# Performance work log

Measured on AMD Instinct MI355X. Metric: run time of the kernel, lower is better.

## Reference

```python
import jax, jax.numpy as jnp
import numpy as np

NEG_SLOPE = 0.2
STRONG_CONVEXITY = 0.5


def _scalar(x, Wq, Wl, bl, Wz, wz_out, wq_out, wl_out):
    # x: [B, D]; Wq/Wl: [L, H, D]; bl: [L, H]; Wz: [L-1, H, H]
    # Precompute all per-layer x-dependent terms in two batched einsums.
    qx = jnp.einsum('lhd,bd->lbh', Wq, x) ** 2          # [L, B, H]
    lx = jnp.einsum('lhd,bd->lbh', Wl, x) + bl[:, None, :]  # [L, B, H]
    z = jax.nn.leaky_relu(qx[0] + lx[0], negative_slope=NEG_SLOPE)

    def step(z, inputs):
        W, q, l = inputs
        z = jax.nn.leaky_relu(z @ W.T + q + l, negative_slope=NEG_SLOPE)
        return z, None

    z, _ = jax.lax.scan(step, z, (Wz, qx[1:], lx[1:]))
    # Final layer to scalar output (no bias on last wx_lin per torch code).
    out = z @ wz_out.T + (x @ wq_out.T) ** 2 + x @ wl_out.T  # [B, 1]
    return out


def setup_inputs() -> dict:
    key = jax.random.key(0)
    ks = jax.random.split(key, 8)
    B, D, H, L = 8192, 128, 512, 10
    f32 = jnp.float32
    x = jax.random.normal(ks[0], (B, D), f32)
    Wq = jax.random.normal(ks[1], (L, H, D), f32) * (1.0 / np.sqrt(D))
    Wl = jax.random.normal(ks[2], (L, H, D), f32) * (1.0 / np.sqrt(D))
    bl = jax.random.normal(ks[3], (L, H), f32) * 0.01
    # wz weights are kept non-negative in the original (clamp/exp init)
    Wz = jnp.abs(jax.random.normal(ks[4], (L - 1, H, H), f32)) * (1.0 / np.sqrt(H))
    wz_out = jnp.abs(jax.random.normal(ks[5], (1, H), f32)) * (1.0 / np.sqrt(H))
    wq_out = jax.random.normal(ks[6], (1, D), f32) * (1.0 / np.sqrt(D))
    wl_out = jax.random.normal(ks[7], (1, D), f32) * (1.0 / np.sqrt(D))
    return {"x": x, "Wq": Wq, "Wl": Wl, "bl": bl, "Wz": Wz,
            "wz_out": wz_out, "wq_out": wq_out, "wl_out": wl_out}


def reference(x, Wq, Wl, bl, Wz, wz_out, wq_out, wl_out):
    # forward = (1 - mu) * d(scalar)/dx + mu * x, with grad_outputs = ones
    def scalar_sum(xx):
        return jnp.sum(_scalar(xx, Wq, Wl, bl, Wz, wz_out, wq_out, wl_out))

    gx = jax.grad(scalar_sum)(x)  # per-sample gradient, [B, D]
    return (1.0 - STRONG_CONVEXITY) * gx + STRONG_CONVEXITY * x
```

## Files before the change

### kernel.cpp

```cpp
#include <hip/hip_runtime.h>


#define Bn 8192
#define Dn 128
#define Hn 512
#define Ln 10
#define NW (Ln * Hn)

constexpr float NS = 0.2f;

typedef __attribute__((ext_vector_type(8))) short short8;
typedef __attribute__((ext_vector_type(4))) float f32x4;

typedef const __attribute__((address_space(1))) void GV;
typedef __attribute__((address_space(3))) void LV;

__device__ __forceinline__ void gload16(const void* g, void* l) {
    __builtin_amdgcn_global_load_lds((GV*)g, (LV*)l, 16, 0, 0);
}

#define MFMA(acc, a, b) acc = __builtin_amdgcn_mfma_f32_16x16x32_bf16(a, b, acc, 0, 0, 0)

__device__ __forceinline__ unsigned short bf16_rne(float v) {
    unsigned u = __float_as_uint(v);
    u += 0x7FFFu + ((u >> 16) & 1u);
    return (unsigned short)(u >> 16);
}
__device__ __forceinline__ float bf2f(unsigned short h) {
    return __uint_as_float(((unsigned)h) << 16);
}
__device__ __forceinline__ void split2(float v, unsigned short& h, unsigned short& l) {
    h = bf16_rne(v);
    l = bf16_rne(v - bf2f(h));
}


__global__ __launch_bounds__(256) void split_flat(const float* __restrict__ in,
        unsigned short* __restrict__ hi, unsigned short* __restrict__ lo, int n4) {
    int i = blockIdx.x * 256 + threadIdx.x;
    if (i >= n4) return;
    float4 v = ((const float4*)in)[i];
    ushort4 h, l;
    split2(v.x, h.x, l.x);
    split2(v.y, h.y, l.y);
    split2(v.z, h.z, l.z);
    split2(v.w, h.w, l.w);
    ((ushort4*)hi)[i] = h;
    ((ushort4*)lo)[i] = l;
}

__global__ __launch_bounds__(256) void transpose_split(const float* __restrict__ in,
        unsigned short* __restrict__ hi, unsigned short* __restrict__ lo, int R, int C) {
    __shared__ float t[32][33];
    const size_t off = (size_t)blockIdx.z * R * C;
    const float* src = in + off;
    unsigned short* dh = hi + off;
    unsigned short* dl = lo + off;
    const int r0 = blockIdx.x * 32, c0 = blockIdx.y * 32;
    const int tr = threadIdx.x >> 5, tc = threadIdx.x & 31;
#pragma unroll
    for (int i = 0; i < 4; ++i)
        t[tr + 8 * i][tc] = src[(size_t)(r0 + tr + 8 * i) * C + c0 + tc];
    __syncthreads();
#pragma unroll
    for (int i = 0; i < 4; ++i) {
        float v = t[tc][tr + 8 * i];
        unsigned short h, l; split2(v, h, l);
        size_t o = (size_t)(c0 + tr + 8 * i) * R + r0 + tc;
        dh[o] = h; dl[o] = l;
    }
}


__global__ __launch_bounds__(256) void gemm_uall(
    const unsigned short* __restrict__ xh, const unsigned short* __restrict__ xl,
    const unsigned short* __restrict__ Wh, const unsigned short* __restrict__ Wv,
    float* __restrict__ u)
{
    __shared__ __align__(16) char smem[32768];
    unsigned short* Ah = (unsigned short*)smem;
    unsigned short* Al = (unsigned short*)(smem + 8192);
    unsigned short* Bh = (unsigned short*)(smem + 16384);
    unsigned short* Bl = (unsigned short*)(smem + 24576);

    const int tid = threadIdx.x;
    const int w = tid >> 6, lane = tid & 63;
    const int lq = lane >> 4, lc = lane & 15;
    const int wm = (w & 1) * 64, wn = (w >> 1) * 64;
    const int row0 = blockIdx.x * 128, col0 = blockIdx.y * 128;
    const int sr = lane >> 2, sk = (lane & 3) * 8;

    f32x4 acc[4][4];
#pragma unroll
    for (int i = 0; i < 4; ++i)
#pragma unroll
        for (int j = 0; j < 4; ++j)
#pragma unroll
            for (int r = 0; r < 4; ++r) acc[i][j][r] = 0.f;

    for (int k0 = 0; k0 < Dn; k0 += 32) {
        __syncthreads();
        for (int c = w; c < 8; c += 4) {
            size_t ga_ = (size_t)(row0 + c * 16 + sr) * Dn + k0 + sk;
            gload16(xh + ga_, Ah + c * 512);
            gload16(xl + ga_, Al + c * 512);
            size_t gb = (size_t)(col0 + c * 16 + sr) * Dn + k0 + sk;
            gload16(Wh + gb, Bh + c * 512);
            gload16(Wv + gb, Bl + c * 512);
        }
        __syncthreads();
        short8 ah[4], al[4];
#pragma unroll
        for (int mt = 0; mt < 4; ++mt) {
            int ao = (wm + mt * 16 + lc) * 32 + lq * 8;
            ah[mt] = *(const short8*)(Ah + ao);
            al[mt] = *(const short8*)(Al + ao);
        }
#pragma unroll
        for (int nt = 0; nt < 4; ++nt) {
            int bo = (wn + nt * 16 + lc) * 32 + lq * 8;
            short8 bh = *(const short8*)(Bh + bo);
            short8 bv = *(const short8*)(Bl + bo);
#pragma unroll
            for (int mt = 0; mt < 4; ++mt) {
                MFMA(acc[mt][nt], ah[mt], bh);
                MFMA(acc[mt][nt], ah[mt], bv);
                MFMA(acc[mt][nt], al[mt], bh);
            }
        }
    }

#pragma unroll
    for (int nt = 0; nt < 4; ++nt) {
        const int col = col0 + wn + nt * 16 + lc;
#pragma unroll
        for (int mt = 0; mt < 4; ++mt) {
            const int rowb = row0 + wm + mt * 16;
#pragma unroll
            for (int r = 0; r < 4; ++r)
                u[(size_t)(rowb + lq * 4 + r) * NW + col] = acc[mt][nt][r];
        }
    }
}


__global__ __launch_bounds__(256) void fwd_mfma(
    const unsigned short* __restrict__ xh, const unsigned short* __restrict__ xl,
    const unsigned short* __restrict__ zph, const unsigned short* __restrict__ zpl,
    const unsigned short* __restrict__ Wzh, const unsigned short* __restrict__ Wzl,
    const unsigned short* __restrict__ Wlh, const unsigned short* __restrict__ Wll,
    const float* __restrict__ bl,
    const float* __restrict__ u,
    unsigned short* __restrict__ zoh, unsigned short* __restrict__ zol,
    unsigned short* __restrict__ mask16, int hasZ)
{
    __shared__ __align__(16) char smem[16384];
    unsigned short* Ah = (unsigned short*)smem;
    unsigned short* Al = (unsigned short*)(smem + 4096);
    unsigned short* Bh = (unsigned short*)(smem + 8192);
    unsigned short* Bl = (unsigned short*)(smem + 12288);

    const int tid = threadIdx.x;
    const int w = tid >> 6, lane = tid & 63;
    const int lq = lane >> 4, lc = lane & 15;
    const int wm = (w & 1) * 32, wn = (w >> 1) * 32;
    const int row0 = blockIdx.x * 64, col0 = blockIdx.y * 64;
    const int sr = lane >> 2, sk = (lane & 3) * 8;

    f32x4 acc[2][2];
#pragma unroll
    for (int i = 0; i < 2; ++i)
#pragma unroll
        for (int j = 0; j < 2; ++j)
#pragma unroll
            for (int r = 0; r < 4; ++r) acc[i][j][r] = 0.f;

    if (hasZ) {
        for (int k0 = 0; k0 < Hn; k0 += 32) {
            __syncthreads();
            {
                size_t ga_ = (size_t)(row0 + w * 16 + sr) * Hn + k0 + sk;
                size_t gb  = (size_t)(col0 + w * 16 + sr) * Hn + k0 + sk;
                gload16(zph + ga_, Ah + w * 512);
                gload16(zpl + ga_, Al + w * 512);
                gload16(Wzh + gb, Bh + w * 512);
                gload16(Wzl + gb, Bl + w * 512);
            }
            __syncthreads();
            short8 ah[2], al[2];
#pragma unroll
            for (int mt = 0; mt < 2; ++mt) {
                int ao = (wm + mt * 16 + lc) * 32 + lq * 8;
                ah[mt] = *(const short8*)(Ah + ao);
                al[mt] = *(const short8*)(Al + ao);
            }
#pragma unroll
            for (int nt = 0; nt < 2; ++nt) {
                int bo = (wn + nt * 16 + lc) * 32 + lq * 8;
                short8 bh = *(const short8*)(Bh + bo);
                short8 bv = *(const short8*)(Bl + bo);
#pragma unroll
                for (int mt = 0; mt < 2; ++mt) {
                    MFMA(acc[mt][nt], ah[mt], bh);
                    MFMA(acc[mt][nt], ah[mt], bv);
                    MFMA(acc[mt][nt], al[mt], bh);
                }
            }
        }
    }

    for (int k0 = 0; k0 < Dn; k0 += 32) {
        __syncthreads();
        {
            size_t ga_ = (size_t)(row0 + w * 16 + sr) * Dn + k0 + sk;
            size_t gb  = (size_t)(col0 + w * 16 + sr) * Dn + k0 + sk;
            gload16(xh + ga_, Ah + w * 512);
            gload16(xl + ga_, Al + w * 512);
            gload16(Wlh + gb, Bh + w * 512);
            gload16(Wll + gb, Bl + w * 512);
        }
        __syncthreads();
        short8 ah[2], al[2];
#pragma unroll
        for (int mt = 0; mt < 2; ++mt) {
            int ao = (wm + mt * 16 + lc) * 32 + lq * 8;
            ah[mt] = *(const short8*)(Ah + ao);
            al[mt] = *(const short8*)(Al + ao);
        }
#pragma unroll
        for (int nt = 0; nt < 2; ++nt) {
            int bo = (wn + nt * 16 + lc) * 32 + lq * 8;
            short8 bh = *(const short8*)(Bh + bo);
            short8 bv = *(const short8*)(Bl + bo);
#pragma unroll
            for (int mt = 0; mt < 2; ++mt) {
                MFMA(acc[mt][nt], ah[mt], bh);
                MFMA(acc[mt][nt], ah[mt], bv);
                MFMA(acc[mt][nt], al[mt], bh);
            }
        }
    }

#pragma unroll
    for (int nt = 0; nt < 2; ++nt) {
        const int colb = col0 + wn + nt * 16;
        const int col = colb + lc;
        const float blv = bl[col];
#pragma unroll
        for (int mt = 0; mt < 2; ++mt) {
            const int rowb = row0 + wm + mt * 16;
#pragma unroll
            for (int r = 0; r < 4; ++r) {
                const int row = rowb + lq * 4 + r;
                float uq = u[(size_t)row * NW + col];
                float pre = acc[mt][nt][r] + uq * uq + blv;
                bool m = pre >= 0.f;
                unsigned long long bal = __ballot(m);
                if (lc == 0) {
                    mask16[(size_t)row * 32 + (colb >> 4)] =
                        (unsigned short)((bal >> (lq * 16)) & 0xFFFFull);
                }
                float zv = m ? pre : NS * pre;
                unsigned short h, l; split2(zv, h, l);
                size_t o = (size_t)row * Hn + col;
                zoh[o] = h; zol[o] = l;
            }
        }
    }
}


__global__ __launch_bounds__(256) void bwd_g_mfma(
    const unsigned short* __restrict__ gah, const unsigned short* __restrict__ gal,
    const unsigned short* __restrict__ WzTh, const unsigned short* __restrict__ WzTl,
    const unsigned short* __restrict__ maskprev,
    const float* __restrict__ u,
    unsigned short* __restrict__ goh, unsigned short* __restrict__ gol,
    unsigned short* __restrict__ a1h, unsigned short* __restrict__ a1l)
{
    __shared__ __align__(16) char smem[16384];
    unsigned short* Ah = (unsigned short*)smem;
    unsigned short* Al = (unsigned short*)(smem + 4096);
    unsigned short* Bh = (unsigned short*)(smem + 8192);
    unsigned short* Bl = (unsigned short*)(smem + 12288);

    const int tid = threadIdx.x;
    const int w = tid >> 6, lane = tid & 63;
    const int lq = lane >> 4, lc = lane & 15;
    const int wm = (w & 1) * 32, wn = (w >> 1) * 32;
    const int row0 = blockIdx.x * 64, col0 = blockIdx.y * 64;
    const int sr = lane >> 2, sk = (lane & 3) * 8;

    f32x4 acc[2][2];
#pragma unroll
    for (int i = 0; i < 2; ++i)
#pragma unroll
        for (int j = 0; j < 2; ++j)
#pragma unroll
            for (int r = 0; r < 4; ++r) acc[i][j][r] = 0.f;

    for (int k0 = 0; k0 < Hn; k0 += 32) {
        __syncthreads();
        {
            size_t ga_ = (size_t)(row0 + w * 16 + sr) * Hn + k0 + sk;
            size_t gb  = (size_t)(col0 + w * 16 + sr) * Hn + k0 + sk;
            gload16(gah + ga_, Ah + w * 512);
            gload16(gal + ga_, Al + w * 512);
            gload16(WzTh + gb, Bh + w * 512);
            gload16(WzTl + gb, Bl + w * 512);
        }
        __syncthreads();
        short8 ah[2], al[2];
#pragma unroll
        for (int mt = 0; mt < 2; ++mt) {
            int ao = (wm + mt * 16 + lc) * 32 + lq * 8;
            ah[mt] = *(const short8*)(Ah + ao);
            al[mt] = *(const short8*)(Al + ao);
        }
#pragma unroll
        for (int nt = 0; nt < 2; ++nt) {
            int bo = (wn + nt * 16 + lc) * 32 + lq * 8;
            short8 bh = *(const short8*)(Bh + bo);
            short8 bv = *(const short8*)(Bl + bo);
#pragma unroll
            for (int mt = 0; mt < 2; ++mt) {
                MFMA(acc[mt][nt], ah[mt], bh);
                MFMA(acc[mt][nt], ah[mt], bv);
                MFMA(acc[mt][nt], al[mt], bh);
            }
        }
    }

#pragma unroll
    for (int nt = 0; nt < 2; ++nt) {
        const int colb = col0 + wn + nt * 16;
        const int col = colb + lc;
#pragma unroll
        for (int mt = 0; mt < 2; ++mt) {
            const int rowb = row0 + wm + mt * 16;
#pragma unroll
            for (int r = 0; r < 4; ++r) {
                int row = rowb + lq * 4 + r;
                unsigned short wbits = maskprev[(size_t)row * 32 + (colb >> 4)];
                float f = ((wbits >> lc) & 1) ? 1.f : NS;
                float v = acc[mt][nt][r] * f;
                unsigned short h, l; split2(v, h, l);
                size_t o = (size_t)row * Hn + col;
                goh[o] = h; gol[o] = l;
                float uv = u[(size_t)row * NW + col];
                float a1 = 2.f * uv * v;
                split2(a1, h, l);
                a1h[o] = h; a1l[o] = l;
            }
        }
    }
}


__global__ __launch_bounds__(256) void bwd_x_mfma(
    const unsigned short* __restrict__ a1h, const unsigned short* __restrict__ a1l,
    const unsigned short* __restrict__ a2h, const unsigned short* __restrict__ a2l,
    const unsigned short* __restrict__ WqTh, const unsigned short* __restrict__ WqTl,
    const unsigned short* __restrict__ WlTh, const unsigned short* __restrict__ WlTl,
    float* __restrict__ gxs)
{
    __shared__ __align__(16) char smem[32768];
    unsigned short* A1h = (unsigned short*)smem;
    unsigned short* A1l = (unsigned short*)(smem + 4096);
    unsigned short* A2h = (unsigned short*)(smem + 8192);
    unsigned short* A2l = (unsigned short*)(smem + 12288);
    unsigned short* Bqh = (unsigned short*)(smem + 16384);
    unsigned short* Bql = (unsigned short*)(smem + 20480);
    unsigned short* Blh = (unsigned short*)(smem + 24576);
    unsigned short* Bll = (unsigned short*)(smem + 28672);

    const int tid = threadIdx.x;
    const int w = tid >> 6, lane = tid & 63;
    const int lq = lane >> 4, lc = lane & 15;
    const int wm = (w & 1) * 32, wn = (w >> 1) * 32;
    const int row0 = blockIdx.x * 64, col0 = blockIdx.y * 64;
    const int kb = blockIdx.z * 256;
    float* gx = gxs + (size_t)blockIdx.z * Bn * Dn;
    const int str = tid >> 2, stk = (tid & 3) * 8;

    f32x4 acc[2][2];
#pragma unroll
    for (int i = 0; i < 2; ++i)
#pragma unroll
        for (int j = 0; j < 2; ++j)
#pragma unroll
            for (int r = 0; r < 4; ++r) acc[i][j][r] = 0.f;

    for (int k0 = kb; k0 < kb + 256; k0 += 32) {
        __syncthreads();
        {
            size_t ga_ = (size_t)(row0 + str) * Hn + k0 + stk;
            size_t gb = (size_t)(col0 + str) * Hn + k0 + stk;
            int lo_ = str * 32 + stk;
            gload16(a1h + ga_, A1h + lo_);
            gload16(a1l + ga_, A1l + lo_);
            gload16(a2h + ga_, A2h + lo_);
            gload16(a2l + ga_, A2l + lo_);
            gload16(WqTh + gb, Bqh + lo_);
            gload16(WqTl + gb, Bql + lo_);
            gload16(WlTh + gb, Blh + lo_);
            gload16(WlTl + gb, Bll + lo_);
        }
        __syncthreads();
        short8 f1h[2], f1l[2], f2h[2], f2l[2];
#pragma unroll
        for (int mt = 0; mt < 2; ++mt) {
            int ao = (wm + mt * 16 + lc) * 32 + lq * 8;
            f1h[mt] = *(const short8*)(A1h + ao);
            f1l[mt] = *(const short8*)(A1l + ao);
            f2h[mt] = *(const short8*)(A2h + ao);
            f2l[mt] = *(const short8*)(A2l + ao);
        }
#pragma unroll
        for (int nt = 0; nt < 2; ++nt) {
            int bo = (wn + nt * 16 + lc) * 32 + lq * 8;
            short8 qh = *(const short8*)(Bqh + bo);
            short8 ql_ = *(const short8*)(Bql + bo);
            short8 lh = *(const short8*)(Blh + bo);
            short8 ll_ = *(const short8*)(Bll + bo);
#pragma unroll
            for (int mt = 0; mt < 2; ++mt) {
                MFMA(acc[mt][nt], f1h[mt], qh);
                MFMA(acc[mt][nt], f1h[mt], ql_);
                MFMA(acc[mt][nt], f1l[mt], qh);
                MFMA(acc[mt][nt], f2h[mt], lh);
                MFMA(acc[mt][nt], f2h[mt], ll_);
                MFMA(acc[mt][nt], f2l[mt], lh);
            }
        }
    }

#pragma unroll
    for (int nt = 0; nt < 2; ++nt) {
        const int col = col0 + wn + nt * 16 + lc;
#pragma unroll
        for (int mt = 0; mt < 2; ++mt) {
            const int rowb = row0 + wm + mt * 16;
#pragma unroll
            for (int r = 0; r < 4; ++r) {
                size_t o = (size_t)(rowb + lq * 4 + r) * Dn + col;
                gx[o] += acc[mt][nt][r];
            }
        }
    }
}


__global__ __launch_bounds__(256) void zero_buf(float* __restrict__ p, int n4) {
    int i = blockIdx.x * 256 + threadIdx.x;
    if (i < n4) ((float4*)p)[i] = make_float4(0.f, 0.f, 0.f, 0.f);
}

__global__ __launch_bounds__(256) void ga_init(
    const float* __restrict__ wz_out, const unsigned short* __restrict__ mask9,
    const float* __restrict__ u9,
    unsigned short* __restrict__ gh, unsigned short* __restrict__ gl,
    unsigned short* __restrict__ a1h, unsigned short* __restrict__ a1l)
{
    int i = blockIdx.x * 256 + threadIdx.x;
    int e = i << 2;
    int b = e >> 9, h = e & 511;
    unsigned short wbits = mask9[(size_t)b * 32 + (h >> 4)];
    float4 wv = *(const float4*)(wz_out + h);
    float4 uv = *(const float4*)(u9 + (size_t)b * NW + h);
    int sh = h & 15;
    ushort4 oh, ol, th, tl;
    float f;
    f = wv.x * (((wbits >> (sh + 0)) & 1) ? 1.f : NS); split2(f, oh.x, ol.x); split2(2.f * uv.x * f, th.x, tl.x);
    f = wv.y * (((wbits >> (sh + 1)) & 1) ? 1.f : NS); split2(f, oh.y, ol.y); split2(2.f * uv.y * f, th.y, tl.y);
    f = wv.z * (((wbits >> (sh + 2)) & 1) ? 1.f : NS); split2(f, oh.z, ol.z); split2(2.f * uv.z * f, th.z, tl.z);
    f = wv.w * (((wbits >> (sh + 3)) & 1) ? 1.f : NS); split2(f, oh.w, ol.w); split2(2.f * uv.w * f, th.w, tl.w);
    *(ushort4*)(gh + e) = oh;
    *(ushort4*)(gl + e) = ol;
    *(ushort4*)(a1h + e) = th;
    *(ushort4*)(a1l + e) = tl;
}

__global__ __launch_bounds__(256) void rowdot_kernel(
    const float* __restrict__ x, const float* __restrict__ wq_out, float* __restrict__ s) {
    const int b = blockIdx.x * 4 + (threadIdx.x >> 6);
    const int lane = threadIdx.x & 63;
    float v = x[(size_t)b * Dn + lane] * wq_out[lane] +
              x[(size_t)b * Dn + 64 + lane] * wq_out[64 + lane];
#pragma unroll
    for (int off = 32; off > 0; off >>= 1) v += __shfl_down(v, off, 64);
    if (lane == 0) s[b] = v;
}

__global__ __launch_bounds__(256) void final_kernel(
    float* __restrict__ out, const float* __restrict__ gxs,
    const float* __restrict__ x, const float* __restrict__ s,
    const float* __restrict__ wq_out, const float* __restrict__ wl_out) {
    const int i = blockIdx.x * 256 + threadIdx.x;
    const int base = i << 2;
    const int b = base >> 7;
    const int d = base & (Dn - 1);
    float4 g0 = *(const float4*)(gxs + base);
    float4 g1 = *(const float4*)(gxs + (size_t)Bn * Dn + base);
    float4 xv = *(const float4*)(x + base);
    float4 wq = *(const float4*)(wq_out + d);
    float4 wl = *(const float4*)(wl_out + d);
    const float sb = s[b];
    float4 o;
    o.x = 0.5f * (g0.x + g1.x) + sb * wq.x + 0.5f * wl.x + 0.5f * xv.x;
    o.y = 0.5f * (g0.y + g1.y) + sb * wq.y + 0.5f * wl.y + 0.5f * xv.y;
    o.z = 0.5f * (g0.z + g1.z) + sb * wq.z + 0.5f * wl.z + 0.5f * xv.z;
    o.w = 0.5f * (g0.w + g1.w) + sb * wq.w + 0.5f * wl.w + 0.5f * xv.w;
    *(float4*)(out + base) = o;
}


extern "C" void kernel_launch(void* const* d_in, const int* in_sizes, int n_in,
                              void* d_out, int out_size, void* d_ws, size_t ws_size,
                              hipStream_t stream) {
    (void)in_sizes; (void)n_in; (void)out_size; (void)ws_size;
    const float* x      = (const float*)d_in[0];
    const float* Wq     = (const float*)d_in[1];
    const float* Wl     = (const float*)d_in[2];
    const float* bl     = (const float*)d_in[3];
    const float* Wz     = (const float*)d_in[4];
    const float* wz_out = (const float*)d_in[5];
    const float* wq_out = (const float*)d_in[6];
    const float* wl_out = (const float*)d_in[7];
    float* out = (float*)d_out;

    char* p = (char*)d_ws;
    #define CARVE(name, bytes) unsigned short* name = (unsigned short*)p; p += (((size_t)(bytes)) + 255) & ~(size_t)255;
    CARVE(xh,  (size_t)Bn*Dn*2)  CARVE(xl,  (size_t)Bn*Dn*2)
    CARVE(Wqh, (size_t)Ln*Hn*Dn*2) CARVE(Wql, (size_t)Ln*Hn*Dn*2)
    CARVE(Wlh, (size_t)Ln*Hn*Dn*2) CARVE(Wll, (size_t)Ln*Hn*Dn*2)
    CARVE(WqTh,(size_t)Ln*Hn*Dn*2) CARVE(WqTl,(size_t)Ln*Hn*Dn*2)
    CARVE(WlTh,(size_t)Ln*Hn*Dn*2) CARVE(WlTl,(size_t)Ln*Hn*Dn*2)
    CARVE(Wzh, (size_t)(Ln-1)*Hn*Hn*2) CARVE(Wzl, (size_t)(Ln-1)*Hn*Hn*2)
    CARVE(WzTh,(size_t)(Ln-1)*Hn*Hn*2) CARVE(WzTl,(size_t)(Ln-1)*Hn*Hn*2)
    CARVE(zAh, (size_t)Bn*Hn*2) CARVE(zAl, (size_t)Bn*Hn*2)
    CARVE(zBh, (size_t)Bn*Hn*2) CARVE(zBl, (size_t)Bn*Hn*2)
    CARVE(a1h, (size_t)Bn*Hn*2) CARVE(a1l, (size_t)Bn*Hn*2)
    CARVE(mask16, (size_t)Ln*Bn*32*2)
    float* s = (float*)p; p += (size_t)Bn*4 + 256;
    float* gxs = (float*)p; p += (size_t)2*Bn*Dn*4;
    float* uall = (float*)p; p += (size_t)Bn*NW*4;
    #undef CARVE

    split_flat<<<(Bn*Dn/4 + 255)/256, 256, 0, stream>>>(x, xh, xl, Bn*Dn/4);
    split_flat<<<(Ln*Hn*Dn/4 + 255)/256, 256, 0, stream>>>(Wq, Wqh, Wql, Ln*Hn*Dn/4);
    split_flat<<<(Ln*Hn*Dn/4 + 255)/256, 256, 0, stream>>>(Wl, Wlh, Wll, Ln*Hn*Dn/4);
    split_flat<<<((Ln-1)*Hn*Hn/4 + 255)/256, 256, 0, stream>>>(Wz, Wzh, Wzl, (Ln-1)*Hn*Hn/4);
    transpose_split<<<dim3(Hn/32, Dn/32, Ln), 256, 0, stream>>>(Wq, WqTh, WqTl, Hn, Dn);
    transpose_split<<<dim3(Hn/32, Dn/32, Ln), 256, 0, stream>>>(Wl, WlTh, WlTl, Hn, Dn);
    transpose_split<<<dim3(Hn/32, Hn/32, Ln-1), 256, 0, stream>>>(Wz, WzTh, WzTl, Hn, Hn);

    rowdot_kernel<<<Bn/4, 256, 0, stream>>>(x, wq_out, s);
    zero_buf<<<(2*Bn*Dn/4 + 255)/256, 256, 0, stream>>>(gxs, 2*Bn*Dn/4);

    gemm_uall<<<dim3(Bn/128, NW/128), 256, 0, stream>>>(xh, xl, Wqh, Wql, uall);

    const dim3 gF(Bn/64, Hn/64);

    fwd_mfma<<<gF, 256, 0, stream>>>(xh, xl, nullptr, nullptr, nullptr, nullptr,
        Wlh, Wll, bl, uall, zAh, zAl, mask16, 0);
    for (int l = 1; l < Ln; ++l) {
        const unsigned short* zh  = (l & 1) ? zAh : zBh;
        const unsigned short* zl_ = (l & 1) ? zAl : zBl;
        unsigned short* oh  = (l & 1) ? zBh : zAh;
        unsigned short* ol_ = (l & 1) ? zBl : zAl;
        fwd_mfma<<<gF, 256, 0, stream>>>(xh, xl, zh, zl_,
            Wzh + (size_t)(l-1)*Hn*Hn, Wzl + (size_t)(l-1)*Hn*Hn,
            Wlh + (size_t)l*Hn*Dn, Wll + (size_t)l*Hn*Dn,
            bl + (size_t)l*Hn, uall + (size_t)l*Hn,
            oh, ol_, mask16 + (size_t)l*Bn*32, 1);
    }

    ga_init<<<(Bn*Hn/4)/256, 256, 0, stream>>>(wz_out, mask16 + (size_t)9*Bn*32,
        uall + (size_t)9*Hn, zAh, zAl, a1h, a1l);

    for (int l = Ln - 1; l >= 0; --l) {
        int sidx = (Ln - 1 - l) & 1;
        const unsigned short* gh_ = sidx ? zBh : zAh;
        const unsigned short* gl_ = sidx ? zBl : zAl;
        bwd_x_mfma<<<dim3(Bn/64, Dn/64, 2), 256, 0, stream>>>(
            a1h, a1l, gh_, gl_,
            WqTh + (size_t)l*Dn*Hn, WqTl + (size_t)l*Dn*Hn,
            WlTh + (size_t)l*Dn*Hn, WlTl + (size_t)l*Dn*Hn, gxs);
        if (l > 0) {
            unsigned short* oh  = sidx ? zAh : zBh;
            unsigned short* ol_ = sidx ? zAl : zBl;
            bwd_g_mfma<<<gF, 256, 0, stream>>>(gh_, gl_,
                WzTh + (size_t)(l-1)*Hn*Hn, WzTl + (size_t)(l-1)*Hn*Hn,
                mask16 + (size_t)(l-1)*Bn*32,
                uall + (size_t)(l-1)*Hn,
                oh, ol_, a1h, a1l);
        }
    }

    final_kernel<<<(Bn*Dn/4)/256, 256, 0, stream>>>(out, gxs, x, s, wq_out, wl_out);
}
```

Measured before the change: 999.0 us.

## Double-buffer LDS tiles in MFMA kernels and skip unused final-layer z writes

Converts the forward, backward-g and backward-x MFMA GEMM loops to a double-buffered LDS scheme. The next K-slice is prefetched with global_load_lds while the current slice is consumed, which drops one barrier per iteration. It also adds a writeZ flag so the last forward layer writes only the mask and skips its z output, which nothing reads. Shared memory per block doubles (up to 64KB in bwd_x), which may lower occupancy. Correctness now relies on the single barrier per iteration being enough for the buffer reuse.

```diff
diff --git a/kernel.cpp b/kernel.cpp
--- a/kernel.cpp
+++ b/kernel.cpp
@@ -152,20 +152,17 @@
     const float* __restrict__ bl,
     const float* __restrict__ u,
     unsigned short* __restrict__ zoh, unsigned short* __restrict__ zol,
-    unsigned short* __restrict__ mask16, int hasZ)
+    unsigned short* __restrict__ mask16, int hasZ, int writeZ)
 {
-    __shared__ __align__(16) char smem[16384];
-    unsigned short* Ah = (unsigned short*)smem;
-    unsigned short* Al = (unsigned short*)(smem + 4096);
-    unsigned short* Bh = (unsigned short*)(smem + 8192);
-    unsigned short* Bl = (unsigned short*)(smem + 12288);
-
+    __shared__ __align__(16) char smem[32768];
+    unsigned short* base = (unsigned short*)smem;
     const int tid = threadIdx.x;
     const int w = tid >> 6, lane = tid & 63;
     const int lq = lane >> 4, lc = lane & 15;
     const int wm = (w & 1) * 32, wn = (w >> 1) * 32;
     const int row0 = blockIdx.x * 64, col0 = blockIdx.y * 64;
     const int sr = lane >> 2, sk = (lane & 3) * 8;
+    const int lA = w * 512;
 
     f32x4 acc[2][2];
 #pragma unroll
@@ -176,29 +173,40 @@
             for (int r = 0; r < 4; ++r) acc[i][j][r] = 0.f;
 
     if (hasZ) {
+        {
+            unsigned short* S = base;
+            size_t ga_ = (size_t)(row0 + w * 16 + sr) * Hn + sk;
+            size_t gb  = (size_t)(col0 + w * 16 + sr) * Hn + sk;
+            gload16(zph + ga_, S + lA);
+            gload16(zpl + ga_, S + 2048 + lA);
+            gload16(Wzh + gb, S + 4096 + lA);
+            gload16(Wzl + gb, S + 6144 + lA);
+        }
+        int cur = 0;
         for (int k0 = 0; k0 < Hn; k0 += 32) {
             __syncthreads();
-            {
-                size_t ga_ = (size_t)(row0 + w * 16 + sr) * Hn + k0 + sk;
-                size_t gb  = (size_t)(col0 + w * 16 + sr) * Hn + k0 + sk;
-                gload16(zph + ga_, Ah + w * 512);
-                gload16(zpl + ga_, Al + w * 512);
-                gload16(Wzh + gb, Bh + w * 512);
-                gload16(Wzl + gb, Bl + w * 512);
-            }
-            __syncthreads();
+            if (k0 + 32 < Hn) {
+                unsigned short* S = base + (cur ^ 1) * 8192;
+                size_t ga_ = (size_t)(row0 + w * 16 + sr) * Hn + k0 + 32 + sk;
+                size_t gb  = (size_t)(col0 + w * 16 + sr) * Hn + k0 + 32 + sk;
+                gload16(zph + ga_, S + lA);
+                gload16(zpl + ga_, S + 2048 + lA);
+                gload16(Wzh + gb, S + 4096 + lA);
+                gload16(Wzl + gb, S + 6144 + lA);
+            }
+            unsigned short* S = base + cur * 8192;
             short8 ah[2], al[2];
 #pragma unroll
             for (int mt = 0; mt < 2; ++mt) {
                 int ao = (wm + mt * 16 + lc) * 32 + lq * 8;
-                ah[mt] = *(const short8*)(Ah + ao);
-                al[mt] = *(const short8*)(Al + ao);
+                ah[mt] = *(const short8*)(S + ao);
+                al[mt] = *(const short8*)(S + 2048 + ao);
             }
 #pragma unroll
             for (int nt = 0; nt < 2; ++nt) {
                 int bo = (wn + nt * 16 + lc) * 32 + lq * 8;
-                short8 bh = *(const short8*)(Bh + bo);
-                short8 bv = *(const short8*)(Bl + bo);
+                short8 bh = *(const short8*)(S + 4096 + bo);
+                short8 bv = *(const short8*)(S + 6144 + bo);
 #pragma unroll
                 for (int mt = 0; mt < 2; ++mt) {
                     MFMA(acc[mt][nt], ah[mt], bh);
@@ -206,32 +214,45 @@
                     MFMA(acc[mt][nt], al[mt], bh);
                 }
             }
-        }
-    }
-
+            cur ^= 1;
+        }
+        __syncthreads();
+    }
+
+    {
+        unsigned short* S = base;
+        size_t ga_ = (size_t)(row0 + w * 16 + sr) * Dn + sk;
+        size_t gb  = (size_t)(col0 + w * 16 + sr) * Dn + sk;
+        gload16(xh + ga_, S + lA);
+        gload16(xl + ga_, S + 2048 + lA);
+        gload16(Wlh + gb, S + 4096 + lA);
+        gload16(Wll + gb, S + 6144 + lA);
+    }
+    int cur = 0;
     for (int k0 = 0; k0 < Dn; k0 += 32) {
         __syncthreads();
-        {
-            size_t ga_ = (size_t)(row0 + w * 16 + sr) * Dn + k0 + sk;
-            size_t gb  = (size_t)(col0 + w * 16 + sr) * Dn + k0 + sk;
-            gload16(xh + ga_, Ah + w * 512);
-            gload16(xl + ga_, Al + w * 512);
-            gload16(Wlh + gb, Bh + w * 512);
-            gload16(Wll + gb, Bl + w * 512);
-        }
-        __syncthreads();
+        if (k0 + 32 < Dn) {
+            unsigned short* S = base + (cur ^ 1) * 8192;
+            size_t ga_ = (size_t)(row0 + w * 16 + sr) * Dn + k0 + 32 + sk;
+            size_t gb  = (size_t)(col0 + w * 16 + sr) * Dn + k0 + 32 + sk;
+            gload16(xh + ga_, S + lA);
+            gload16(xl + ga_, S + 2048 + lA);
+            gload16(Wlh + gb, S + 4096 + lA);
+            gload16(Wll + gb, S + 6144 + lA);
+        }
+        unsigned short* S = base + cur * 8192;
         short8 ah[2], al[2];
 #pragma unroll
         for (int mt = 0; mt < 2; ++mt) {
             int ao = (wm + mt * 16 + lc) * 32 + lq * 8;
-            ah[mt] = *(const short8*)(Ah + ao);
-            al[mt] = *(const short8*)(Al + ao);
+            ah[mt] = *(const short8*)(S + ao);
+            al[mt] = *(const short8*)(S + 2048 + ao);
         }
 #pragma unroll
         for (int nt = 0; nt < 2; ++nt) {
             int bo = (wn + nt * 16 + lc) * 32 + lq * 8;
-            short8 bh = *(const short8*)(Bh + bo);
-            short8 bv = *(const short8*)(Bl + bo);
+            short8 bh = *(const short8*)(S + 4096 + bo);
+            short8 bv = *(const short8*)(S + 6144 + bo);
 #pragma unroll
             for (int mt = 0; mt < 2; ++mt) {
                 MFMA(acc[mt][nt], ah[mt], bh);
@@ -239,6 +260,7 @@
                 MFMA(acc[mt][nt], al[mt], bh);
             }
         }
+        cur ^= 1;
     }
 
 #pragma unroll
@@ -260,10 +282,12 @@
                     mask16[(size_t)row * 32 + (colb >> 4)] =
                         (unsigned short)((bal >> (lq * 16)) & 0xFFFFull);
                 }
-                float zv = m ? pre : NS * pre;
-                unsigned short h, l; split2(zv, h, l);
-                size_t o = (size_t)row * Hn + col;
-                zoh[o] = h; zol[o] = l;
+                if (writeZ) {
+                    float zv = m ? pre : NS * pre;
+                    unsigned short h, l; split2(zv, h, l);
+                    size_t o = (size_t)row * Hn + col;
+                    zoh[o] = h; zol[o] = l;
+                }
             }
         }
     }
@@ -278,18 +302,15 @@
     unsigned short* __restrict__ goh, unsigned short* __restrict__ gol,
     unsigned short* __restrict__ a1h, unsigned short* __restrict__ a1l)
 {
-    __shared__ __align__(16) char smem[16384];
-    unsigned short* Ah = (unsigned short*)smem;
-    unsigned short* Al = (unsigned short*)(smem + 4096);
-    unsigned short* Bh = (unsigned short*)(smem + 8192);
-    unsigned short* Bl = (unsigned short*)(smem + 12288);
-
+    __shared__ __align__(16) char smem[32768];
+    unsigned short* base = (unsigned short*)smem;
     const int tid = threadIdx.x;
     const int w = tid >> 6, lane = tid & 63;
     const int lq = lane >> 4, lc = lane & 15;
     const int wm = (w & 1) * 32, wn = (w >> 1) * 32;
     const int row0 = blockIdx.x * 64, col0 = blockIdx.y * 64;
     const int sr = lane >> 2, sk = (lane & 3) * 8;
+    const int lA = w * 512;
 
     f32x4 acc[2][2];
 #pragma unroll
@@ -299,29 +320,40 @@
 #pragma unroll
             for (int r = 0; r < 4; ++r) acc[i][j][r] = 0.f;
 
+    {
+        unsigned short* S = base;
+        size_t ga_ = (size_t)(row0 + w * 16 + sr) * Hn + sk;
+        size_t gb  = (size_t)(col0 + w * 16 + sr) * Hn + sk;
+        gload16(gah + ga_, S + lA);
+        gload16(gal + ga_, S + 2048 + lA);
+        gload16(WzTh + gb, S + 4096 + lA);
+        gload16(WzTl + gb, S + 6144 + lA);
+    }
+    int cur = 0;
     for (int k0 = 0; k0 < Hn; k0 += 32) {
         __syncthreads();
-        {
-            size_t ga_ = (size_t)(row0 + w * 16 + sr) * Hn + k0 + sk;
-            size_t gb  = (size_t)(col0 + w * 16 + sr) * Hn + k0 + sk;
-            gload16(gah + ga_, Ah + w * 512);
-            gload16(gal + ga_, Al + w * 512);
-            gload16(WzTh + gb, Bh + w * 512);
-            gload16(WzTl + gb, Bl + w * 512);
-        }
-        __syncthreads();
+        if (k0 + 32 < Hn) {
+            unsigned short* S = base + (cur ^ 1) * 8192;
+            size_t ga_ = (size_t)(row0 + w * 16 + sr) * Hn + k0 + 32 + sk;
+            size_t gb  = (size_t)(col0 + w * 16 + sr) * Hn + k0 + 32 + sk;
+            gload16(gah + ga_, S + lA);
+            gload16(gal + ga_, S + 2048 + lA);
+            gload16(WzTh + gb, S + 4096 + lA);
+            gload16(WzTl + gb, S + 6144 + lA);
+        }
+        unsigned short* S = base + cur * 8192;
         short8 ah[2], al[2];
 #pragma unroll
         for (int mt = 0; mt < 2; ++mt) {
             int ao = (wm + mt * 16 + lc) * 32 + lq * 8;
-            ah[mt] = *(const short8*)(Ah + ao);
-            al[mt] = *(const short8*)(Al + ao);
+            ah[mt] = *(const short8*)(S + ao);
+            al[mt] = *(const short8*)(S + 2048 + ao);
         }
 #pragma unroll
         for (int nt = 0; nt < 2; ++nt) {
             int bo = (wn + nt * 16 + lc) * 32 + lq * 8;
-            short8 bh = *(const short8*)(Bh + bo);
-            short8 bv = *(const short8*)(Bl + bo);
+            short8 bh = *(const short8*)(S + 4096 + bo);
+            short8 bv = *(const short8*)(S + 6144 + bo);
 #pragma unroll
             for (int mt = 0; mt < 2; ++mt) {
                 MFMA(acc[mt][nt], ah[mt], bh);
@@ -329,6 +361,7 @@
                 MFMA(acc[mt][nt], al[mt], bh);
             }
         }
+        cur ^= 1;
     }
 
 #pragma unroll
@@ -364,16 +397,8 @@
     const unsigned short* __restrict__ WlTh, const unsigned short* __restrict__ WlTl,
     float* __restrict__ gxs)
 {
-    __shared__ __align__(16) char smem[32768];
-    unsigned short* A1h = (unsigned short*)smem;
-    unsigned short* A1l = (unsigned short*)(smem + 4096);
-    unsigned short* A2h = (unsigned short*)(smem + 8192);
-    unsigned short* A2l = (unsigned short*)(smem + 12288);
-    unsigned short* Bqh = (unsigned short*)(smem + 16384);
-    unsigned short* Bql = (unsigned short*)(smem + 20480);
-    unsigned short* Blh = (unsigned short*)(smem + 24576);
-    unsigned short* Bll = (unsigned short*)(smem + 28672);
-
+    __shared__ __align__(16) char smem[65536];
+    unsigned short* base = (unsigned short*)smem;
     const int tid = threadIdx.x;
     const int w = tid >> 6, lane = tid & 63;
     const int lq = lane >> 4, lc = lane & 15;
@@ -381,7 +406,8 @@
     const int row0 = blockIdx.x * 64, col0 = blockIdx.y * 64;
     const int kb = blockIdx.z * 256;
     float* gx = gxs + (size_t)blockIdx.z * Bn * Dn;
-    const int str = tid >> 2, stk = (tid & 3) * 8;
+    const int sr = lane >> 2, sk = (lane & 3) * 8;
+    const int lA = w * 512;
 
     f32x4 acc[2][2];
 #pragma unroll
@@ -391,38 +417,52 @@
 #pragma unroll
             for (int r = 0; r < 4; ++r) acc[i][j][r] = 0.f;
 
+    {
+        unsigned short* S = base;
+        size_t ga_ = (size_t)(row0 + w * 16 + sr) * Hn + kb + sk;
+        size_t gb  = (size_t)(col0 + w * 16 + sr) * Hn + kb + sk;
+        gload16(a1h + ga_, S + lA);
+        gload16(a1l + ga_, S + 2048 + lA);
+        gload16(a2h + ga_, S + 4096 + lA);
+        gload16(a2l + ga_, S + 6144 + lA);
+        gload16(WqTh + gb, S + 8192 + lA);
+        gload16(WqTl + gb, S + 10240 + lA);
+        gload16(WlTh + gb, S + 12288 + lA);
+        gload16(WlTl + gb, S + 14336 + lA);
+    }
+    int cur = 0;
     for (int k0 = kb; k0 < kb + 256; k0 += 32) {
         __syncthreads();
-        {
-            size_t ga_ = (size_t)(row0 + str) * Hn + k0 + stk;
-            size_t gb = (size_t)(col0 + str) * Hn + k0 + stk;
-            int lo_ = str * 32 + stk;
-            gload16(a1h + ga_, A1h + lo_);
-            gload16(a1l + ga_, A1l + lo_);
-            gload16(a2h + ga_, A2h + lo_);
-            gload16(a2l + ga_, A2l + lo_);
-            gload16(WqTh + gb, Bqh + lo_);
-            gload16(WqTl + gb, Bql + lo_);
-            gload16(WlTh + gb, Blh + lo_);
-            gload16(WlTl + gb, Bll + lo_);
-        }
-        __syncthreads();
+        if (k0 + 32 < kb + 256) {
+            unsigned short* S = base + (cur ^ 1) * 16384;
+            size_t ga_ = (size_t)(row0 + w * 16 + sr) * Hn + k0 + 32 + sk;
+            size_t gb  = (size_t)(col0 + w * 16 + sr) * Hn + k0 + 32 + sk;
+            gload16(a1h + ga_, S + lA);
+            gload16(a1l + ga_, S + 2048 + lA);
+            gload16(a2h + ga_, S + 4096 + lA);
+            gload16(a2l + ga_, S + 6144 + lA);
+            gload16(WqTh + gb, S + 8192 + lA);
+            gload16(WqTl + gb, S + 10240 + lA);
+            gload16(WlTh + gb, S + 12288 + lA);
+            gload16(WlTl + gb, S + 14336 + lA);
+        }
+        unsigned short* S = base + cur * 16384;
         short8 f1h[2], f1l[2], f2h[2], f2l[2];
 #pragma unroll
         for (int mt = 0; mt < 2; ++mt) {
             int ao = (wm + mt * 16 + lc) * 32 + lq * 8;
-            f1h[mt] = *(const short8*)(A1h + ao);
-            f1l[mt] = *(const short8*)(A1l + ao);
-            f2h[mt] = *(const short8*)(A2h + ao);
-            f2l[mt] = *(const short8*)(A2l + ao);
+            f1h[mt] = *(const short8*)(S + ao);
+            f1l[mt] = *(const short8*)(S + 2048 + ao);
+            f2h[mt] = *(const short8*)(S + 4096 + ao);
+            f2l[mt] = *(const short8*)(S + 6144 + ao);
         }
 #pragma unroll
         for (int nt = 0; nt < 2; ++nt) {
             int bo = (wn + nt * 16 + lc) * 32 + lq * 8;
-            short8 qh = *(const short8*)(Bqh + bo);
-            short8 ql_ = *(const short8*)(Bql + bo);
-            short8 lh = *(const short8*)(Blh + bo);
-            short8 ll_ = *(const short8*)(Bll + bo);
+            short8 qh = *(const short8*)(S + 8192 + bo);
+            short8 ql_ = *(const short8*)(S + 10240 + bo);
+            short8 lh = *(const short8*)(S + 12288 + bo);
+            short8 ll_ = *(const short8*)(S + 14336 + bo);
 #pragma unroll
             for (int mt = 0; mt < 2; ++mt) {
                 MFMA(acc[mt][nt], f1h[mt], qh);
@@ -433,6 +473,7 @@
                 MFMA(acc[mt][nt], f2l[mt], lh);
             }
         }
+        cur ^= 1;
     }
 
 #pragma unroll
@@ -563,7 +604,7 @@
     const dim3 gF(Bn/64, Hn/64);
 
     fwd_mfma<<<gF, 256, 0, stream>>>(xh, xl, nullptr, nullptr, nullptr, nullptr,
-        Wlh, Wll, bl, uall, zAh, zAl, mask16, 0);
+        Wlh, Wll, bl, uall, zAh, zAl, mask16, 0, 1);
     for (int l = 1; l < Ln; ++l) {
         const unsigned short* zh  = (l & 1) ? zAh : zBh;
         const unsigned short* zl_ = (l & 1) ? zAl : zBl;
@@ -573,7 +614,7 @@
             Wzh + (size_t)(l-1)*Hn*Hn, Wzl + (size_t)(l-1)*Hn*Hn,
             Wlh + (size_t)l*Hn*Dn, Wll + (size_t)l*Hn*Dn,
             bl + (size_t)l*Hn, uall + (size_t)l*Hn,
-            oh, ol_, mask16 + (size_t)l*Bn*32, 1);
+            oh, ol_, mask16 + (size_t)l*Bn*32, 1, (l < Ln - 1) ? 1 : 0);
     }
 
     ga_init<<<(Bn*Hn/4)/256, 256, 0, stream>>>(wz_out, mask16 + (size_t)9*Bn*32,
```

Measured after the change: 1.060 ms. 6.1% more time.
